# Kernel optimization log

Measured on AMD Instinct MI355X. Metric: run time of the kernel, lower is better.

The kernel has to match this reference:

```python
import jax, jax.numpy as jnp
import numpy as np

N, E, G = 50000, 1600000, 512
IN_DIM, HEADS, C1, C2, HIDDEN = 128, 3, 32, 32, 512
NEG_SLOPE = 0.2
EPS = 1e-16


def _glorot(key, shape):
    fan_in = shape[0]
    return jax.random.normal(key, shape, dtype=jnp.float32) / np.sqrt(fan_in)


def setup_inputs() -> dict:
    key = jax.random.key(0)
    ks = jax.random.split(key, 16)
    x = jax.random.normal(ks[0], (N, IN_DIM), dtype=jnp.float32)
    edge_index = jax.random.randint(ks[1], (2, E), 0, N, dtype=jnp.int64)
    batch = (jnp.arange(N, dtype=jnp.int64) * G) // N  # sorted, all graphs non-empty
    d1, d2 = HEADS * C1, HEADS * C2
    return {
        "x": x,
        "W_l1": _glorot(ks[2], (IN_DIM, d1)), "b_l1": jnp.zeros((d1,), jnp.float32),
        "W_r1": _glorot(ks[3], (IN_DIM, d1)), "b_r1": jnp.zeros((d1,), jnp.float32),
        "att1": _glorot(ks[4], (HEADS, C1)), "bias1": jnp.zeros((d1,), jnp.float32),
        "W_l2": _glorot(ks[5], (d1, d2)), "b_l2": jnp.zeros((d2,), jnp.float32),
        "W_r2": _glorot(ks[6], (d1, d2)), "b_r2": jnp.zeros((d2,), jnp.float32),
        "att2": _glorot(ks[7], (HEADS, C2)), "bias2": jnp.zeros((d2,), jnp.float32),
        "W_fc1": _glorot(ks[8], (d1 + d2, HIDDEN)), "b_fc1": jnp.zeros((HIDDEN,), jnp.float32),
        "W_fc2": _glorot(ks[9], (HIDDEN, 2)), "b_fc2": jnp.zeros((2,), jnp.float32),
        "edge_index": edge_index,
        "batch": batch,
    }


def gatv2_conv(xin, src, dst, W_l, b_l, W_r, b_r, att, bias, heads, out_c):
    n = xin.shape[0]
    x_l = (xin @ W_l + b_l).reshape(n, heads, out_c)  # source-side projection
    x_r = (xin @ W_r + b_r).reshape(n, heads, out_c)  # target-side projection
    e = jax.nn.leaky_relu(x_l[src] + x_r[dst], NEG_SLOPE)  # [E', H, C]
    logits = jnp.einsum("ehc,hc->eh", e, att)  # [E', H]
    m = jax.ops.segment_max(logits, dst, num_segments=n)
    a = jnp.exp(logits - m[dst])
    denom = jax.ops.segment_sum(a, dst, num_segments=n)
    alpha = a / (denom[dst] + EPS)  # per-destination edge softmax (PyG semantics)
    out = jax.ops.segment_sum(x_l[src] * alpha[:, :, None], dst, num_segments=n)
    return out.reshape(n, heads * out_c) + bias


def reference(x, W_l1, b_l1, W_r1, b_r1, att1, bias1,
              W_l2, b_l2, W_r2, b_r2, att2, bias2,
              W_fc1, b_fc1, W_fc2, b_fc2, edge_index, batch):
    n = x.shape[0]
    loop = jnp.arange(n, dtype=edge_index.dtype)
    src = jnp.concatenate([edge_index[0], loop])  # PyG GATv2Conv adds self-loops
    dst = jnp.concatenate([edge_index[1], loop])
    h1 = jnp.tanh(gatv2_conv(x, src, dst, W_l1, b_l1, W_r1, b_r1, att1, bias1, HEADS, C1))
    h2 = jnp.tanh(gatv2_conv(h1, src, dst, W_l2, b_l2, W_r2, b_r2, att2, bias2, HEADS, C2))
    h = jnp.concatenate([h1, h2], axis=1)  # [N, (C1+C2)*H]
    first_idx = jnp.searchsorted(batch, jnp.arange(G, dtype=batch.dtype))  # first node of each graph
    pooled = h[first_idx]  # [G, (C1+C2)*H]
    hidden = jax.nn.relu(pooled @ W_fc1 + b_fc1)
    logits = hidden @ W_fc2 + b_fc2
    return jax.nn.log_softmax(logits, axis=1)
```

## Files before the change

### kernel.cpp

```cpp
#include <hip/hip_runtime.h>
#include <hip/hip_bf16.h>
#include <hip/hip_fp16.h>
#include <math.h>

#define NN 50000
#define EE 1600000
#define GG 512
#define INDIM 128
#define HEADS 3
#define CC 32
#define DD 96
#define HID 512
#define NEG 0.2f
#define NEGM1 (NEG - 1.0f)
#define EPS_DEN 1e-16f
#define CAP 128
#define NBW 1568
#define LOG2E 1.44269504f
#define PCLAMP2 86.5617f

#define PS_BL1   0
#define PS_BR1   96
#define PS_ATT1  192
#define PS_BIAS1 288
#define PS_BL2   384
#define PS_BR2   480
#define PS_ATT2  576
#define PS_BIAS2 672
#define PS_BFC1  768
#define PS_WFC2  1280
#define PS_BFC2  2304
#define PS_TOTAL 2308

typedef _Float16 h8 __attribute__((ext_vector_type(8)));
typedef float f4 __attribute__((ext_vector_type(4)));

static __device__ __forceinline__ float bf2f(__hip_bfloat16 v) { return __bfloat162float(v); }

static __device__ __forceinline__ int getI(const void* p, long long i, bool w64) {
    return w64 ? ((const int*)p)[2 * i] : ((const int*)p)[i];
}

static __device__ __forceinline__ float rawf(const void* p, int i, bool isbf) {
    return isbf ? bf2f(((const __hip_bfloat16*)p)[i]) : ((const float*)p)[i];
}

static __device__ __forceinline__ void load4(const void* p, int base, int e0, bool w64, int* v) {
    const int4* q = (const int4*)p;
    if (w64) {
        int4 a = q[(base + e0) >> 1];
        int4 b = q[((base + e0) >> 1) + 1];
        v[0] = a.x; v[1] = a.z; v[2] = b.x; v[3] = b.z;
    } else {
        int4 a = q[(base + e0) >> 2];
        v[0] = a.x; v[1] = a.y; v[2] = a.z; v[3] = a.w;
    }
}

static __device__ __forceinline__ bool testbit(const unsigned* b, int i) {
    return (b[i >> 5] >> (i & 31)) & 1u;
}

template <int CTRL>
static __device__ __forceinline__ float dpp_add(float v) {
    int t = __builtin_amdgcn_update_dpp(0, __float_as_int(v), CTRL, 0xF, 0xF, true);
    return v + __int_as_float(t);
}
static __device__ __forceinline__ float red16(float p) {
    p = dpp_add<0x121>(p);
    p = dpp_add<0x122>(p);
    p = dpp_add<0x124>(p);
    p = dpp_add<0x128>(p);
    return p;
}

static __device__ __forceinline__ float edge_e(float2 x, float2 xr2, float2 aa) {
    float t0 = x.x + xr2.x; t0 = fmaf(fminf(t0, 0.0f), NEGM1, t0);
    float t1 = x.y + xr2.y; t1 = fmaf(fminf(t1, 0.0f), NEGM1, t1);
    return exp2f(fminf(red16(fmaf(t1, aa.y, t0 * aa.x)), PCLAMP2));
}

__global__ void detect_kernel(const void* __restrict__ x, const void* __restrict__ ei,
                              int* __restrict__ flags)
{
    __shared__ int wild, zcnt;
    if (threadIdx.x == 0) { wild = 0; zcnt = 0; }
    __syncthreads();
    int w = 0, z = 0;
    const __hip_bfloat16* xb = (const __hip_bfloat16*)x;
    for (int i = threadIdx.x; i < 4096; i += 256) {
        float v = bf2f(xb[i]);
        if (!(fabsf(v) <= 1e6f)) w++;
    }
    const int* e32 = (const int*)ei;
    for (int i = threadIdx.x; i < 4096; i += 256) {
        if (e32[2 * i + 1] == 0) z++;
    }
    atomicAdd(&wild, w);
    atomicAdd(&zcnt, z);
    __syncthreads();
    if (threadIdx.x == 0) {
        flags[0] = (wild < 64) ? 1 : 0;
        flags[1] = (zcnt > 4000) ? 1 : 0;
    }
}

struct SetupArgs {
    const void *wl1, *wr1, *wl2, *wr2, *wfc1;
    const void *bl1, *br1, *att1, *bias1, *bl2, *br2, *att2, *bias2, *bfc1, *wfc2, *bfc2;
    const void *batch;
};

__global__ void setup_kernel(SetupArgs a, const int* __restrict__ flags,
                             float* __restrict__ P, __half* __restrict__ B1,
                             __half* __restrict__ B2, __half* __restrict__ Bfc,
                             int* __restrict__ deg, int* __restrict__ needed,
                             int* __restrict__ first, unsigned* __restrict__ pb,
                             int* __restrict__ cnt)
{
    const int task = blockIdx.y;
    const int idx = blockIdx.x * 256 + threadIdx.x;
    const bool isbf = flags[0] != 0;

    if (task == 0) {
        if (idx == 0) *cnt = 0;
        if (idx >= PS_TOTAL) return;
        const void* src; int rel;
        if (idx < 768) {
            int k = idx / 96; rel = idx - k * 96;
            const void* s8[8] = {a.bl1, a.br1, a.att1, a.bias1, a.bl2, a.br2, a.att2, a.bias2};
            src = s8[k];
        } else if (idx < 1280) { src = a.bfc1; rel = idx - 768; }
        else if (idx < 2304)   { src = a.wfc2; rel = idx - 1280; }
        else if (idx < 2306)   { src = a.bfc2; rel = idx - 2304; }
        else return;
        P[idx] = rawf(src, rel, isbf);
    } else if (task == 1 || task == 2) {
        const int KC = (task == 1) ? 4 : 3;
        const int total = 12 * KC * 64;
        if (idx >= total) return;
        int lane = idx & 63, t = idx >> 6;
        int kc = t % KC, ntile = t / KC;
        int n = ntile * 16 + (lane & 15);
        int kbase = kc * 32 + (lane >> 4) * 8;
        const void* W = (task == 1) ? (n < 96 ? a.wl1 : a.wr1) : (n < 96 ? a.wl2 : a.wr2);
        int n2 = (n < 96) ? n : n - 96;
        __half* dst = ((task == 1) ? B1 : B2) + (size_t)idx * 8;
#pragma unroll
        for (int j = 0; j < 8; j++) dst[j] = __float2half(rawf(W, (kbase + j) * 96 + n2, isbf));
    } else if (task == 3) {
        const int total = 32 * 6 * 64;
        if (idx >= total) return;
        int lane = idx & 63, t = idx >> 6;
        int kc = t % 6, ntile = t / 6;
        int n = ntile * 16 + (lane & 15);
        int kbase = kc * 32 + (lane >> 4) * 8;
        __half* dst = Bfc + (size_t)idx * 8;
#pragma unroll
        for (int j = 0; j < 8; j++) dst[j] = __float2half(rawf(a.wfc1, (kbase + j) * HID + n, isbf));
    } else if (task == 4) {
        int i0 = idx * 4;
#pragma unroll
        for (int j = 0; j < 4; j++) if (i0 + j < NN) deg[i0 + j] = 0;
    } else if (task == 5) {
        if (idx >= NN) return;
        const bool w64 = flags[1] != 0;
        int b = getI(a.batch, idx, w64);
        bool isf = (idx == 0) || (getI(a.batch, idx - 1, w64) != b);
        needed[idx] = isf ? 1 : 0;
        if (isf) first[b] = idx;
    } else {
        if (idx >= NBW) return;
        const bool w64 = flags[1] != 0;
        unsigned word = 0;
        int prev = (idx == 0) ? -1 : getI(a.batch, idx * 32 - 1, w64);
        for (int bit = 0; bit < 32; bit++) {
            int i = idx * 32 + bit;
            if (i >= NN) break;
            int b = getI(a.batch, i, w64);
            if (i == 0 || b != prev) word |= (1u << bit);
            prev = b;
        }
        pb[idx] = word;
    }
}

__global__ void mark_needed_kernel(const void* __restrict__ ei, const int* __restrict__ flags,
                                   const unsigned* __restrict__ pb, int* __restrict__ needed)
{
    int e0 = (blockIdx.x * 256 + threadIdx.x) * 4;
    if (e0 >= EE) return;
    const bool w64 = flags[1] != 0;
    int d4[4];
    load4(ei, EE, e0, w64, d4);
#pragma unroll
    for (int j = 0; j < 4; j++)
        if (testbit(pb, d4[j])) needed[getI(ei, e0 + j, w64)] = 1;
}

template <int KDIM, int MODE>
static __device__ __forceinline__ void proj_body(
    int bx, const void* __restrict__ Ain, const __half* __restrict__ Bg,
    const int* __restrict__ list, const int* __restrict__ cnt,
    const float* __restrict__ P, const int* __restrict__ flags, int offBl, int offBr,
    __half* __restrict__ xl, float* __restrict__ xr)
{
    constexpr int KC = KDIM / 32;
    const int tid = threadIdx.x;
    const int limit = MODE ? *cnt : NN;
    const int wave = tid >> 6;
    const int lane = tid & 63;
    const int base = bx * 64 + wave * 16;
    if (base >= limit) return;

    const int q = lane >> 4;
    const int mlane = lane & 15;

    int aIdx = base + mlane;
    int aRow;
    if (MODE) aRow = (aIdx < limit) ? list[aIdx] : list[limit - 1];
    else      aRow = (aIdx < limit) ? aIdx : 0;

    h8 a[KC];
    if (MODE == 1) {
        const h8* arow = reinterpret_cast<const h8*>((const __half*)Ain + (size_t)aRow * KDIM);
#pragma unroll
        for (int kc = 0; kc < KC; kc++) a[kc] = arow[kc * 4 + q];
    } else if (flags[0]) {
        const int4* arow = reinterpret_cast<const int4*>((const ushort*)Ain + (size_t)aRow * KDIM);
#pragma unroll
        for (int kc = 0; kc < KC; kc++) {
            int4 r = arow[kc * 4 + q];
            int ws[4] = {r.x, r.y, r.z, r.w};
#pragma unroll
            for (int i = 0; i < 4; i++) {
                a[kc][2 * i]     = (_Float16)__int_as_float(ws[i] << 16);
                a[kc][2 * i + 1] = (_Float16)__int_as_float(ws[i] & 0xffff0000);
            }
        }
    } else {
        const f4* arow = reinterpret_cast<const f4*>((const float*)Ain + (size_t)aRow * KDIM);
#pragma unroll
        for (int kc = 0; kc < KC; kc++) {
            f4 r0 = arow[kc * 8 + q * 2];
            f4 r1 = arow[kc * 8 + q * 2 + 1];
#pragma unroll
            for (int i = 0; i < 4; i++) {
                a[kc][i]     = (_Float16)r0[i];
                a[kc][4 + i] = (_Float16)r1[i];
            }
        }
    }

    int sRow[4];
#pragma unroll
    for (int r = 0; r < 4; r++) {
        int si = base + q * 4 + r;
        sRow[r] = (si < limit) ? (MODE ? list[si] : si) : -1;
    }

    const h8* Bf = reinterpret_cast<const h8*>(Bg);
#pragma unroll
    for (int ntile = 0; ntile < 12; ntile++) {
        int n = ntile * 16 + mlane;
        float bv = (n < 96) ? P[offBl + n] : P[offBr + n - 96];
        f4 acc = {bv, bv, bv, bv};
#pragma unroll
        for (int kc = 0; kc < KC; kc++) {
            h8 b = Bf[(ntile * KC + kc) * 64 + lane];
            acc = __builtin_amdgcn_mfma_f32_16x16x32_f16(a[kc], b, acc, 0, 0, 0);
        }
#pragma unroll
        for (int r = 0; r < 4; r++) {
            if (sRow[r] < 0) continue;
            if (n < 96) xl[(size_t)sRow[r] * DD + n] = __float2half(acc[r]);
            else        xr[(size_t)sRow[r] * DD + (n - 96)] = acc[r];
        }
    }
}

__global__ __launch_bounds__(256) void mid_kernel(
    const void* __restrict__ ei, const int* __restrict__ flags,
    const int* __restrict__ needed,
    int* __restrict__ deg, int* __restrict__ csr,
    int* __restrict__ list, int* __restrict__ cnt,
    const void* __restrict__ x, const __half* __restrict__ B1,
    const float* __restrict__ P, __half* __restrict__ xl, float* __restrict__ xr)
{
    const int slice = blockIdx.y;
    if (slice == 2) {
        proj_body<INDIM, 0>(blockIdx.x, x, B1, nullptr, nullptr, P, flags,
                            PS_BL1, PS_BR1, xl, xr);
        return;
    }
    if (slice == 1) {
        int i = blockIdx.x * 256 + threadIdx.x;
        if (i >= NN) return;
        if (needed[i]) list[atomicAdd(cnt, 1)] = i;
        return;
    }
    int e0 = (blockIdx.x * 256 + threadIdx.x) * 4;
    if (e0 >= EE) return;
    const bool w64 = flags[1] != 0;
    int s4[4], d4[4];
    load4(ei, EE, e0, w64, d4);
    int nd0 = needed[d4[0]], nd1 = needed[d4[1]], nd2 = needed[d4[2]], nd3 = needed[d4[3]];
    if (!(nd0 | nd1 | nd2 | nd3)) return;
    load4(ei, 0, e0, w64, s4);
    int nd[4] = {nd0, nd1, nd2, nd3};
#pragma unroll
    for (int j = 0; j < 4; j++) {
        int dst = d4[j];
        if (!nd[j]) continue;
        int pos = atomicAdd(&deg[dst], 1);
        if (pos < CAP) csr[(size_t)dst * CAP + pos] = s4[j] * (DD / 2);
    }
}

template <int KDIM, int MODE>
__global__ __launch_bounds__(256) void proj_g_kernel(
    const void* __restrict__ Ain, const __half* __restrict__ Bg,
    const int* __restrict__ list, const int* __restrict__ cnt,
    const float* __restrict__ P, const int* __restrict__ flags, int offBl, int offBr,
    __half* __restrict__ xl, float* __restrict__ xr)
{
    proj_body<KDIM, MODE>(blockIdx.x, Ain, Bg, list, cnt, P, flags, offBl, offBr, xl, xr);
}

template <int OUTMODE>
__global__ __launch_bounds__(256) void fused_edge_kernel(
    const int* __restrict__ csr, const int* __restrict__ deg,
    const int* __restrict__ list, const int* __restrict__ cnt,
    const __half* __restrict__ xl, const float* __restrict__ xr,
    const float* __restrict__ P, int offAtt, int offBias,
    __half* __restrict__ out)
{
    const int lane = threadIdx.x & 63;
    const int g = lane >> 4;
    const int t = lane & 15;
    const int w0 = (blockIdx.x * 256 + threadIdx.x) >> 6;
    const int nw = (gridDim.x * 256) >> 6;
    const int limit = (OUTMODE == 0) ? *cnt : GG;
    const __half2* xl2p = reinterpret_cast<const __half2*>(xl);

    float2 a_[3];
#pragma unroll
    for (int h = 0; h < 3; h++) {
        float2 av = *reinterpret_cast<const float2*>(P + offAtt + h * CC + 2 * t);
        a_[h].x = av.x * LOG2E; a_[h].y = av.y * LOG2E;
    }

    for (int li = w0; li < limit; li += nw) {
        const int n = list[li];
        const int* row = csr + (size_t)n * CAP;
        const int end = min(deg[n], CAP);
        const float* xrn = xr + (size_t)n * DD;
        float2 xr_[3];
#pragma unroll
        for (int h = 0; h < 3; h++) xr_[h] = *reinterpret_cast<const float2*>(xrn + h * CC + 2 * t);

        float d0, d1, d2, o00, o01, o10, o11, o20, o21;
        {
            const __half2* sp = xl2p + n * (DD / 2) + t;
            float2 x0 = __half22float2(sp[0]);
            float2 x1 = __half22float2(sp[16]);
            float2 x2 = __half22float2(sp[32]);
            float e0 = edge_e(x0, xr_[0], a_[0]);
            float e1 = edge_e(x1, xr_[1], a_[1]);
            float e2 = edge_e(x2, xr_[2], a_[2]);
            if (g == 0) {
                d0 = e0; o00 = e0 * x0.x; o01 = e0 * x0.y;
                d1 = e1; o10 = e1 * x1.x; o11 = e1 * x1.y;
                d2 = e2; o20 = e2 * x2.x; o21 = e2 * x2.y;
            } else {
                d0 = d1 = d2 = 0.0f;
                o00 = o01 = o10 = o11 = o20 = o21 = 0.0f;
            }
        }

        int k = g;
        for (; k + 12 < end; k += 16) {
            int s0 = row[k], s1 = row[k + 4], s2 = row[k + 8], s3 = row[k + 12];
            const __half2* p0 = xl2p + s0 + t;
            const __half2* p1 = xl2p + s1 + t;
            const __half2* p2 = xl2p + s2 + t;
            const __half2* p3 = xl2p + s3 + t;
            __half2 r00 = p0[0], r01 = p0[16], r02 = p0[32];
            __half2 r10 = p1[0], r11 = p1[16], r12 = p1[32];
            __half2 r20 = p2[0], r21 = p2[16], r22 = p2[32];
            __half2 r30 = p3[0], r31 = p3[16], r32 = p3[32];
            float2 xa0 = __half22float2(r00), xa1 = __half22float2(r01), xa2 = __half22float2(r02);
            float2 xb0 = __half22float2(r10), xb1 = __half22float2(r11), xb2 = __half22float2(r12);
            float2 xc0 = __half22float2(r20), xc1 = __half22float2(r21), xc2 = __half22float2(r22);
            float2 xd0 = __half22float2(r30), xd1 = __half22float2(r31), xd2 = __half22float2(r32);
            float ea0 = edge_e(xa0, xr_[0], a_[0]), ea1 = edge_e(xa1, xr_[1], a_[1]), ea2 = edge_e(xa2, xr_[2], a_[2]);
            float eb0 = edge_e(xb0, xr_[0], a_[0]), eb1 = edge_e(xb1, xr_[1], a_[1]), eb2 = edge_e(xb2, xr_[2], a_[2]);
            float ec0 = edge_e(xc0, xr_[0], a_[0]), ec1 = edge_e(xc1, xr_[1], a_[1]), ec2 = edge_e(xc2, xr_[2], a_[2]);
            float ed0 = edge_e(xd0, xr_[0], a_[0]), ed1 = edge_e(xd1, xr_[1], a_[1]), ed2 = edge_e(xd2, xr_[2], a_[2]);
            d0 += (ea0 + eb0) + (ec0 + ed0);
            d1 += (ea1 + eb1) + (ec1 + ed1);
            d2 += (ea2 + eb2) + (ec2 + ed2);
            o00 = fmaf(ea0, xa0.x, o00); o00 = fmaf(eb0, xb0.x, o00); o00 = fmaf(ec0, xc0.x, o00); o00 = fmaf(ed0, xd0.x, o00);
            o01 = fmaf(ea0, xa0.y, o01); o01 = fmaf(eb0, xb0.y, o01); o01 = fmaf(ec0, xc0.y, o01); o01 = fmaf(ed0, xd0.y, o01);
            o10 = fmaf(ea1, xa1.x, o10); o10 = fmaf(eb1, xb1.x, o10); o10 = fmaf(ec1, xc1.x, o10); o10 = fmaf(ed1, xd1.x, o10);
            o11 = fmaf(ea1, xa1.y, o11); o11 = fmaf(eb1, xb1.y, o11); o11 = fmaf(ec1, xc1.y, o11); o11 = fmaf(ed1, xd1.y, o11);
            o20 = fmaf(ea2, xa2.x, o20); o20 = fmaf(eb2, xb2.x, o20); o20 = fmaf(ec2, xc2.x, o20); o20 = fmaf(ed2, xd2.x, o20);
            o21 = fmaf(ea2, xa2.y, o21); o21 = fmaf(eb2, xb2.y, o21); o21 = fmaf(ec2, xc2.y, o21); o21 = fmaf(ed2, xd2.y, o21);
        }
        for (; k + 4 < end; k += 8) {
            int s0 = row[k], s1 = row[k + 4];
            const __half2* p0 = xl2p + s0 + t;
            const __half2* p1 = xl2p + s1 + t;
            __half2 ra0 = p0[0], ra1 = p0[16], ra2 = p0[32];
            __half2 rb0 = p1[0], rb1 = p1[16], rb2 = p1[32];
            float2 xa0 = __half22float2(ra0), xa1 = __half22float2(ra1), xa2 = __half22float2(ra2);
            float2 xb0 = __half22float2(rb0), xb1 = __half22float2(rb1), xb2 = __half22float2(rb2);
            float ea0 = edge_e(xa0, xr_[0], a_[0]), ea1 = edge_e(xa1, xr_[1], a_[1]), ea2 = edge_e(xa2, xr_[2], a_[2]);
            float eb0 = edge_e(xb0, xr_[0], a_[0]), eb1 = edge_e(xb1, xr_[1], a_[1]), eb2 = edge_e(xb2, xr_[2], a_[2]);
            d0 += ea0 + eb0; d1 += ea1 + eb1; d2 += ea2 + eb2;
            o00 = fmaf(ea0, xa0.x, o00); o00 = fmaf(eb0, xb0.x, o00);
            o01 = fmaf(ea0, xa0.y, o01); o01 = fmaf(eb0, xb0.y, o01);
            o10 = fmaf(ea1, xa1.x, o10); o10 = fmaf(eb1, xb1.x, o10);
            o11 = fmaf(ea1, xa1.y, o11); o11 = fmaf(eb1, xb1.y, o11);
            o20 = fmaf(ea2, xa2.x, o20); o20 = fmaf(eb2, xb2.x, o20);
            o21 = fmaf(ea2, xa2.y, o21); o21 = fmaf(eb2, xb2.y, o21);
        }
        for (; k < end; k += 4) {
            int s0 = row[k];
            const __half2* p0 = xl2p + s0 + t;
            float2 xa0 = __half22float2(p0[0]);
            float2 xa1 = __half22float2(p0[16]);
            float2 xa2 = __half22float2(p0[32]);
            float ea0 = edge_e(xa0, xr_[0], a_[0]);
            float ea1 = edge_e(xa1, xr_[1], a_[1]);
            float ea2 = edge_e(xa2, xr_[2], a_[2]);
            d0 += ea0; d1 += ea1; d2 += ea2;
            o00 = fmaf(ea0, xa0.x, o00); o01 = fmaf(ea0, xa0.y, o01);
            o10 = fmaf(ea1, xa1.x, o10); o11 = fmaf(ea1, xa1.y, o11);
            o20 = fmaf(ea2, xa2.x, o20); o21 = fmaf(ea2, xa2.y, o21);
        }

        d0 += __shfl_xor(d0, 16); d0 += __shfl_xor(d0, 32);
        d1 += __shfl_xor(d1, 16); d1 += __shfl_xor(d1, 32);
        d2 += __shfl_xor(d2, 16); d2 += __shfl_xor(d2, 32);
        o00 += __shfl_xor(o00, 16); o00 += __shfl_xor(o00, 32);
        o01 += __shfl_xor(o01, 16); o01 += __shfl_xor(o01, 32);
        o10 += __shfl_xor(o10, 16); o10 += __shfl_xor(o10, 32);
        o11 += __shfl_xor(o11, 16); o11 += __shfl_xor(o11, 32);
        o20 += __shfl_xor(o20, 16); o20 += __shfl_xor(o20, 32);
        o21 += __shfl_xor(o21, 16); o21 += __shfl_xor(o21, 32);

        if (g == 0) {
            float inv0 = 1.0f / (d0 + EPS_DEN);
            float inv1 = 1.0f / (d1 + EPS_DEN);
            float inv2 = 1.0f / (d2 + EPS_DEN);
            float2 bv0 = *reinterpret_cast<const float2*>(P + offBias + 0 * CC + 2 * t);
            float2 bv1 = *reinterpret_cast<const float2*>(P + offBias + 1 * CC + 2 * t);
            float2 bv2 = *reinterpret_cast<const float2*>(P + offBias + 2 * CC + 2 * t);
            __half2 h0 = __floats2half2_rn(tanhf(fmaf(o00, inv0, bv0.x)), tanhf(fmaf(o01, inv0, bv0.y)));
            __half2 h1 = __floats2half2_rn(tanhf(fmaf(o10, inv1, bv1.x)), tanhf(fmaf(o11, inv1, bv1.y)));
            __half2 h2 = __floats2half2_rn(tanhf(fmaf(o20, inv2, bv2.x)), tanhf(fmaf(o21, inv2, bv2.y)));
            __half* ob = (OUTMODE == 0) ? (out + (size_t)n * DD) : (out + (size_t)li * DD);
            *reinterpret_cast<__half2*>(ob + 0 * CC + 2 * t) = h0;
            *reinterpret_cast<__half2*>(ob + 1 * CC + 2 * t) = h1;
            *reinterpret_cast<__half2*>(ob + 2 * CC + 2 * t) = h2;
        }
    }
}

__global__ __launch_bounds__(256) void mlp_mfma_kernel(
    const __half* __restrict__ h1h, const __half* __restrict__ A2,
    const int* __restrict__ first, const __half* __restrict__ Bfc,
    const float* __restrict__ P, const int* __restrict__ flags, void* __restrict__ outv)
{
    const int tid = threadIdx.x;
    const int wave = tid >> 6, lane = tid & 63;
    const int q = lane >> 4, ml = lane & 15;
    const int rowbase = blockIdx.x * 64 + wave * 16;
    const int g16 = rowbase + ml;

    h8 a[6];
    {
        const h8* l = reinterpret_cast<const h8*>(h1h + (size_t)first[g16] * DD);
#pragma unroll
        for (int kc = 0; kc < 3; kc++) a[kc] = l[kc * 4 + q];
        const h8* r = reinterpret_cast<const h8*>(A2 + (size_t)g16 * DD);
#pragma unroll
        for (int kc = 3; kc < 6; kc++) a[kc] = r[(kc - 3) * 4 + q];
    }

    const h8* Bf = reinterpret_cast<const h8*>(Bfc);
    const float* w2 = P + PS_WFC2;
    float p0[4] = {0, 0, 0, 0}, p1[4] = {0, 0, 0, 0};
    for (int nt = 0; nt < 32; nt++) {
        int n = nt * 16 + ml;
        float bv = P[PS_BFC1 + n];
        f4 acc = {bv, bv, bv, bv};
#pragma unroll
        for (int kc = 0; kc < 6; kc++)
            acc = __builtin_amdgcn_mfma_f32_16x16x32_f16(a[kc], Bf[(nt * 6 + kc) * 64 + lane], acc, 0, 0, 0);
        float w20 = w2[2 * n], w21 = w2[2 * n + 1];
#pragma unroll
        for (int r = 0; r < 4; r++) {
            float hdn = fmaxf(acc[r], 0.0f);
            p0[r] = fmaf(hdn, w20, p0[r]);
            p1[r] = fmaf(hdn, w21, p1[r]);
        }
    }
#pragma unroll
    for (int off = 1; off <= 8; off <<= 1) {
#pragma unroll
        for (int r = 0; r < 4; r++) {
            p0[r] += __shfl_xor(p0[r], off);
            p1[r] += __shfl_xor(p1[r], off);
        }
    }
    if (ml == 0) {
        float b0 = P[PS_BFC2], b1 = P[PS_BFC2 + 1];
#pragma unroll
        for (int r = 0; r < 4; r++) {
            int g = rowbase + q * 4 + r;
            float l0 = p0[r] + b0, l1 = p1[r] + b1;
            float mx = fmaxf(l0, l1);
            float lse = mx + logf(__expf(l0 - mx) + __expf(l1 - mx));
            if (flags[0]) {
                ((__hip_bfloat16*)outv)[g * 2 + 0] = __float2bfloat16(l0 - lse);
                ((__hip_bfloat16*)outv)[g * 2 + 1] = __float2bfloat16(l1 - lse);
            } else {
                ((float*)outv)[g * 2 + 0] = l0 - lse;
                ((float*)outv)[g * 2 + 1] = l1 - lse;
            }
        }
    }
}

extern "C" void kernel_launch(void* const* d_in, const int* in_sizes, int n_in,
                              void* d_out, int out_size, void* d_ws, size_t ws_size,
                              hipStream_t stream)
{
    const void* x     = d_in[0];
    const void* ei    = d_in[17];
    const void* batch = d_in[18];

    float* ws   = (float*)d_ws;
    float* P    = ws;
    float* xr   = P + PS_TOTAL;

    __half* hp   = (__half*)(xr + (size_t)NN * DD);
    __half* xlh  = hp;
    __half* xl2h = xlh + (size_t)NN * DD;
    __half* h1h  = xl2h + (size_t)NN * DD;
    __half* A2   = h1h + (size_t)NN * DD;
    __half* B1   = A2 + (size_t)GG * DD;
    __half* B2   = B1 + 24576;
    __half* Bfc  = B2 + 18432;

    int* ip       = (int*)(Bfc + 98304);
    int* deg      = ip;
    int* needed   = deg + NN;
    int* cnt      = needed + NN;
    int* csr      = cnt + 4;
    int* list     = csr + (size_t)NN * CAP;
    int* first    = list + NN;
    int* flags    = first + GG;
    unsigned* pb  = (unsigned*)(flags + 4);

    SetupArgs sa;
    sa.wl1 = d_in[1];  sa.bl1 = d_in[2];  sa.wr1 = d_in[3];  sa.br1 = d_in[4];
    sa.att1 = d_in[5]; sa.bias1 = d_in[6];
    sa.wl2 = d_in[7];  sa.bl2 = d_in[8];  sa.wr2 = d_in[9];  sa.br2 = d_in[10];
    sa.att2 = d_in[11]; sa.bias2 = d_in[12];
    sa.wfc1 = d_in[13]; sa.bfc1 = d_in[14]; sa.wfc2 = d_in[15]; sa.bfc2 = d_in[16];
    sa.batch = batch;

    const int edge4B = (EE / 4 + 255) / 256;
    const int mprojB = (NN + 63) / 64;
    const int fuse1B = 2048;
    const int fuse2B = GG / 4;

    detect_kernel<<<1, 256, 0, stream>>>(x, ei, flags);
    setup_kernel<<<dim3(196, 7), 256, 0, stream>>>(sa, flags, P, B1, B2, Bfc,
                                                   deg, needed, first, pb, cnt);
    mark_needed_kernel<<<edge4B, 256, 0, stream>>>(ei, flags, pb, needed);

    mid_kernel<<<dim3(edge4B, 3), 256, 0, stream>>>(ei, flags, needed, deg, csr, list, cnt,
                                                    x, B1, P, xlh, xr);

    fused_edge_kernel<0><<<fuse1B, 256, 0, stream>>>(csr, deg, list, cnt, xlh, xr,
                                                     P, PS_ATT1, PS_BIAS1, h1h);

    proj_g_kernel<DD, 1><<<mprojB, 256, 0, stream>>>(h1h, B2, list, cnt,
                                                     P, flags, PS_BL2, PS_BR2, xl2h, xr);
    fused_edge_kernel<1><<<fuse2B, 256, 0, stream>>>(csr, deg, first, nullptr, xl2h, xr,
                                                     P, PS_ATT2, PS_BIAS2, A2);

    mlp_mfma_kernel<<<GG / 64, 256, 0, stream>>>(h1h, A2, first, Bfc, P, flags, d_out);
}
```

Measured before the change: 254.0 us.

## Replace int needed array with bitmask and build node list per word

The per-node int 'needed' flags become a packed bitmask set with atomicOr, cleared in the detect kernel. The mark kernel now handles 16 edges per thread and loads source indices only when a destination hits. The list builder walks bitmask words with popc and ffs, using one atomic per word instead of one per node. This cuts memory traffic and random int lookups, at the cost of atomicOr contention on shared words and a list order that still depends on atomic timing.

```diff
diff --git a/kernel.cpp b/kernel.cpp
--- a/kernel.cpp
+++ b/kernel.cpp
@@ -81,11 +81,12 @@
 }
 
 __global__ void detect_kernel(const void* __restrict__ x, const void* __restrict__ ei,
-                              int* __restrict__ flags)
+                              int* __restrict__ flags, unsigned* __restrict__ nb)
 {
     __shared__ int wild, zcnt;
     if (threadIdx.x == 0) { wild = 0; zcnt = 0; }
     __syncthreads();
+    for (int i = threadIdx.x; i < NBW; i += 256) nb[i] = 0;
     int w = 0, z = 0;
     const __hip_bfloat16* xb = (const __hip_bfloat16*)x;
     for (int i = threadIdx.x; i < 4096; i += 256) {
@@ -114,7 +115,7 @@
 __global__ void setup_kernel(SetupArgs a, const int* __restrict__ flags,
                              float* __restrict__ P, __half* __restrict__ B1,
                              __half* __restrict__ B2, __half* __restrict__ Bfc,
-                             int* __restrict__ deg, int* __restrict__ needed,
+                             int* __restrict__ deg, unsigned* __restrict__ nb,
                              int* __restrict__ first, unsigned* __restrict__ pb,
                              int* __restrict__ cnt)
 {
@@ -167,8 +168,10 @@
         const bool w64 = flags[1] != 0;
         int b = getI(a.batch, idx, w64);
         bool isf = (idx == 0) || (getI(a.batch, idx - 1, w64) != b);
-        needed[idx] = isf ? 1 : 0;
-        if (isf) first[b] = idx;
+        if (isf) {
+            first[b] = idx;
+            atomicOr(&nb[idx >> 5], 1u << (idx & 31));
+        }
     } else {
         if (idx >= NBW) return;
         const bool w64 = flags[1] != 0;
@@ -186,16 +189,28 @@
 }
 
 __global__ void mark_needed_kernel(const void* __restrict__ ei, const int* __restrict__ flags,
-                                   const unsigned* __restrict__ pb, int* __restrict__ needed)
-{
-    int e0 = (blockIdx.x * 256 + threadIdx.x) * 4;
+                                   const unsigned* __restrict__ pb, unsigned* __restrict__ nb)
+{
+    int e0 = (blockIdx.x * 256 + threadIdx.x) * 16;
     if (e0 >= EE) return;
     const bool w64 = flags[1] != 0;
-    int d4[4];
-    load4(ei, EE, e0, w64, d4);
-#pragma unroll
-    for (int j = 0; j < 4; j++)
-        if (testbit(pb, d4[j])) needed[getI(ei, e0 + j, w64)] = 1;
+    int d[16];
+#pragma unroll
+    for (int q = 0; q < 4; q++) load4(ei, EE, e0 + q * 4, w64, d + q * 4);
+    unsigned hit = 0;
+#pragma unroll
+    for (int j = 0; j < 16; j++)
+        if (testbit(pb, d[j])) hit |= (1u << j);
+    if (!hit) return;
+#pragma unroll
+    for (int q = 0; q < 4; q++) {
+        if (!((hit >> (q * 4)) & 0xF)) continue;
+        int s[4];
+        load4(ei, 0, e0 + q * 4, w64, s);
+#pragma unroll
+        for (int j = 0; j < 4; j++)
+            if ((hit >> (q * 4 + j)) & 1) atomicOr(&nb[s[j] >> 5], 1u << (s[j] & 31));
+    }
 }
 
 template <int KDIM, int MODE>
@@ -281,7 +296,7 @@
 
 __global__ __launch_bounds__(256) void mid_kernel(
     const void* __restrict__ ei, const int* __restrict__ flags,
-    const int* __restrict__ needed,
+    const unsigned* __restrict__ nb,
     int* __restrict__ deg, int* __restrict__ csr,
     int* __restrict__ list, int* __restrict__ cnt,
     const void* __restrict__ x, const __half* __restrict__ B1,
@@ -294,24 +309,36 @@
         return;
     }
     if (slice == 1) {
-        int i = blockIdx.x * 256 + threadIdx.x;
-        if (i >= NN) return;
-        if (needed[i]) list[atomicAdd(cnt, 1)] = i;
+        int wdi = blockIdx.x * 256 + threadIdx.x;
+        if (wdi >= NBW) return;
+        unsigned w = nb[wdi];
+        if (!w) return;
+        int c = __popc(w);
+        int base = atomicAdd(cnt, c);
+        int node = wdi * 32;
+        while (w) {
+            int b = __ffs(w) - 1;
+            list[base++] = node + b;
+            w &= w - 1;
+        }
         return;
     }
     int e0 = (blockIdx.x * 256 + threadIdx.x) * 4;
     if (e0 >= EE) return;
     const bool w64 = flags[1] != 0;
-    int s4[4], d4[4];
+    int d4[4];
     load4(ei, EE, e0, w64, d4);
-    int nd0 = needed[d4[0]], nd1 = needed[d4[1]], nd2 = needed[d4[2]], nd3 = needed[d4[3]];
-    if (!(nd0 | nd1 | nd2 | nd3)) return;
+    unsigned hit = 0;
+#pragma unroll
+    for (int j = 0; j < 4; j++)
+        if (testbit(nb, d4[j])) hit |= (1u << j);
+    if (!hit) return;
+    int s4[4];
     load4(ei, 0, e0, w64, s4);
-    int nd[4] = {nd0, nd1, nd2, nd3};
 #pragma unroll
     for (int j = 0; j < 4; j++) {
+        if (!((hit >> j) & 1)) continue;
         int dst = d4[j];
-        if (!nd[j]) continue;
         int pos = atomicAdd(&deg[dst], 1);
         if (pos < CAP) csr[(size_t)dst * CAP + pos] = s4[j] * (DD / 2);
     }
@@ -557,13 +584,13 @@
 
     int* ip       = (int*)(Bfc + 98304);
     int* deg      = ip;
-    int* needed   = deg + NN;
-    int* cnt      = needed + NN;
+    int* cnt      = deg + NN;
     int* csr      = cnt + 4;
     int* list     = csr + (size_t)NN * CAP;
     int* first    = list + NN;
     int* flags    = first + GG;
     unsigned* pb  = (unsigned*)(flags + 4);
+    unsigned* nb  = pb + NBW;
 
     SetupArgs sa;
     sa.wl1 = d_in[1];  sa.bl1 = d_in[2];  sa.wr1 = d_in[3];  sa.br1 = d_in[4];
@@ -574,16 +601,17 @@
     sa.batch = batch;
 
     const int edge4B = (EE / 4 + 255) / 256;
+    const int edge16B = (EE / 16 + 255) / 256;
     const int mprojB = (NN + 63) / 64;
     const int fuse1B = 2048;
     const int fuse2B = GG / 4;
 
-    detect_kernel<<<1, 256, 0, stream>>>(x, ei, flags);
+    detect_kernel<<<1, 256, 0, stream>>>(x, ei, flags, nb);
     setup_kernel<<<dim3(196, 7), 256, 0, stream>>>(sa, flags, P, B1, B2, Bfc,
-                                                   deg, needed, first, pb, cnt);
-    mark_needed_kernel<<<edge4B, 256, 0, stream>>>(ei, flags, pb, needed);
-
-    mid_kernel<<<dim3(edge4B, 3), 256, 0, stream>>>(ei, flags, needed, deg, csr, list, cnt,
+                                                   deg, nb, first, pb, cnt);
+    mark_needed_kernel<<<edge16B, 256, 0, stream>>>(ei, flags, pb, nb);
+
+    mid_kernel<<<dim3(edge4B, 3), 256, 0, stream>>>(ei, flags, nb, deg, csr, list, cnt,
                                                     x, B1, P, xlh, xr);
 
     fused_edge_kernel<0><<<fuse1B, 256, 0, stream>>>(csr, deg, list, cnt, xlh, xr,
```

Result: no change. 250.1 us (-1.5%).
